# Performance work log

Measured on AMD Instinct MI355X. Metric: run time of the kernel, lower is better.

Reference implementation:

```python
import jax, jax.numpy as jnp
import numpy as np

_FIRST_DECODE_ID = 0  # _T5_DECODER_START_TOKEN_ID
B, L, V = 1, 520, 32128
REVIEW_INDEX = 512
LENIENCY = 2


def setup_inputs() -> dict:
    key = jax.random.key(0)
    k1, k2, k3 = jax.random.split(key, 3)
    target_logits = jax.random.normal(k1, (B, L, V), dtype=jnp.float32)
    probs = jax.random.uniform(k2, (B, L, V), dtype=jnp.float32)
    input_ids = jax.random.randint(k3, (B, L), 0, V, dtype=jnp.int64)
    return {
        "target_logits": target_logits,
        "probs": probs,
        "input_ids": input_ids,
        "review_index": REVIEW_INDEX,
        "leniency": LENIENCY,
    }


def reference(target_logits, probs, input_ids, review_index, leniency):
    r = int(review_index)
    L = input_ids.shape[1]
    K = L - r  # number of draft tokens under review

    target_probs = jax.nn.softmax(target_logits, axis=-1)          # (1, L, V)
    argmax_ids = jnp.argmax(target_probs, axis=-1)                  # (1, L)
    first = jnp.full((1, 1), _FIRST_DECODE_ID, dtype=input_ids.dtype)
    target_ids = jnp.concatenate([first, argmax_ids.astype(input_ids.dtype)], axis=-1)[:, r:]  # (1, K+1)
    target_probs_s = target_probs[:, r - 1:, :]                     # (1, K+1, V)
    probs_new = probs[:, r - 1:, :]                                 # (1, K+1, V)
    draft_ids = input_ids[:, r:]                                    # (1, K)

    # verification flags (fused replacement of the python early-exit loop)
    eq = target_ids[:, :K] == draft_ids                             # (1, K)
    tp = jnp.take_along_axis(target_probs_s[:, :K, :], draft_ids[..., None], axis=-1)[..., 0]
    pp = jnp.take_along_axis(probs_new[:, :K, :], draft_ids[..., None], axis=-1)[..., 0]
    lenient = (leniency > 1) & (tp > pp / jnp.float32(leniency))
    accept = eq | lenient                                           # (1, K)
    # n_match = length of leading run of accepts == match_ct in the loop
    n_match = jnp.sum(jnp.cumprod(accept.astype(jnp.int32), axis=-1))

    # id_res: prefix (r) + accepted drafts (n_match) + 1 bonus target token, padded to r+K+1
    pos = jnp.arange(K + 1)
    draft_pad = jnp.pad(draft_ids, ((0, 0), (0, 1)))                # (1, K+1)
    new_ids = jnp.where(pos < n_match, draft_pad[0],
                        jnp.where(pos == n_match, target_ids[0], 0))
    id_res = jnp.concatenate([input_ids[0, :r], new_ids])[None, :]  # (1, r+K+1)

    # prob_res: probs[:, :r] ++ target_probs of accepted positions, zero-padded to r+K
    mask = (jnp.arange(K) < n_match)[:, None]
    new_probs = jnp.where(mask, target_probs_s[0, :K, :], jnp.float32(0.0))
    prob_res = jnp.concatenate([probs[0, :r, :], new_probs], axis=0)[None]  # (1, r+K, V)

    return id_res, prob_res, n_match
```

## Files before the change

kernel.cpp:

```cpp
#include <hip/hip_runtime.h>
#include <hip/hip_bf16.h>


#define NCHUNK 32
#define BLK 256
#define KFIX 8
#define NSTATS ((KFIX + 1) * NCHUNK)

struct Ws {
    float pmax[16][NCHUNK];
    float psum[16][NCHUNK];
    int   pidx[16][NCHUNK];
};

struct MIS { float m; int i; float s; };

__device__ inline MIS mis_merge(MIS a, MIS b) {
    MIS r;
    r.i = (b.m > a.m || (b.m == a.m && b.i < a.i)) ? b.i : a.i;
    r.m = fmaxf(a.m, b.m);
    r.s = 0.0f;
    if (a.s > 0.0f) r.s += a.s * expf(a.m - r.m);
    if (b.s > 0.0f) r.s += b.s * expf(b.m - r.m);
    return r;
}

typedef float f4  __attribute__((ext_vector_type(4)));
typedef float f4u __attribute__((ext_vector_type(4), aligned(4)));

__global__ __launch_bounds__(BLK)
void stats_kernel(const float* __restrict__ logits, Ws* __restrict__ ws, int V, int r) {
    __shared__ float sm[BLK];
    __shared__ int   si[BLK];
    __shared__ float ss[BLK];
    int t = threadIdx.x;
    int b = blockIdx.x;

    int ch = b & (NCHUNK - 1);
    int j  = b / NCHUNK;
    int chunk_elems = V / NCHUNK;
    int cf4 = chunk_elems / 4;
    int cbase = ch * chunk_elems;
    const float4* row = (const float4*)(logits + (size_t)(r - 1 + j) * V + cbase);

    float m = -INFINITY, s = 0.0f;
    int   mi = 0x7fffffff;
    for (int f = t; f < cf4; f += BLK) {
        float4 v = row[f];
        float vv[4] = {v.x, v.y, v.z, v.w};
        int c = cbase + f * 4;
        #pragma unroll
        for (int u = 0; u < 4; u++) {
            float x = vv[u];
            if (x > m) { s = s * expf(m - x) + 1.0f; m = x; mi = c + u; }
            else       { s += expf(x - m); }
        }
    }
    sm[t] = m; si[t] = mi; ss[t] = s;
    __syncthreads();
    for (int w = BLK >> 1; w > 0; w >>= 1) {
        if (t < w) {
            MIS a = {sm[t], si[t], ss[t]};
            MIS bb = {sm[t + w], si[t + w], ss[t + w]};
            MIS rr = mis_merge(a, bb);
            sm[t] = rr.m; si[t] = rr.i; ss[t] = rr.s;
        }
        __syncthreads();
    }
    if (t == 0) {
        ws->pmax[j][ch] = sm[0];
        ws->psum[j][ch] = ss[0];
        ws->pidx[j][ch] = si[0];
    }
}

__global__ __launch_bounds__(BLK)
void spec_kernel(const float* __restrict__ logits, const float* __restrict__ probs,
                 const int* __restrict__ ids, const int* __restrict__ leniency_p,
                 float* __restrict__ out, const Ws* __restrict__ ws,
                 int V, int r, int K, long long prob_off, long long out_last) {
    __shared__ float s_mx[12];
    __shared__ float s_sum[12];
    __shared__ int   s_amax[12];
    __shared__ int   s_draft[12];
    __shared__ int   s_acc[12];
    __shared__ int   s_nm;
    int t = threadIdx.x;
    int b = blockIdx.x;

    if (t <= K) {
        MIS acc = {ws->pmax[t][0], ws->pidx[t][0], ws->psum[t][0]};
        for (int c = 1; c < NCHUNK; c++) {
            MIS bb = {ws->pmax[t][c], ws->pidx[t][c], ws->psum[t][c]};
            acc = mis_merge(acc, bb);
        }
        s_mx[t] = acc.m; s_sum[t] = acc.s; s_amax[t] = acc.i;
    }
    __syncthreads();
    if (t < K) {
        int dj = ids[r + t];
        s_draft[t] = dj;
        size_t rowoff = (size_t)(r - 1 + t) * V;
        float tp = expf(logits[rowoff + dj] - s_mx[t]) / s_sum[t];
        float pp = probs[rowoff + dj];
        int   len = *leniency_p;
        bool eq      = (s_amax[t] == dj);
        bool lenient = (len > 1) && (tp > pp / (float)len);
        s_acc[t] = (eq || lenient) ? 1 : 0;
    }
    __syncthreads();
    if (t == 0) {
        int nm = 0;
        for (int q = 0; q < K; q++) { if (s_acc[q]) nm++; else break; }
        s_nm = nm;
    }
    __syncthreads();
    int nm = s_nm;

    if (b < 32) {
        int j = b >> 2, sub = b & 3;
        long long ob = prob_off + (long long)(r + j) * V;
        const float* lg = logits + (size_t)(r - 1 + j) * V;
        bool on = (j < nm);
        float m   = s_mx[j];
        float inv = on ? (1.0f / s_sum[j]) : 0.0f;
        if (sub == 0) {
            if (t < 3)       out[ob + t]     = on ? expf(lg[t] - m) * inv : 0.0f;
            else if (t == 3) out[ob + V - 1] = on ? expf(lg[V - 1] - m) * inv : 0.0f;
        }
        int nf4r = (V - 4) / 4;
        int i0 = sub * 2008;
        int i1 = i0 + 2008; if (i1 > nf4r) i1 = nf4r;
        float* dst = out + ob + 3;
        const float* srcl = lg + 3;
        for (int i = i0 + t; i < i1; i += BLK) {
            f4 v;
            if (on) {
                f4u x = *reinterpret_cast<const f4u*>(srcl + 4 * (size_t)i);
                v.x = expf(x.x - m) * inv; v.y = expf(x.y - m) * inv;
                v.z = expf(x.z - m) * inv; v.w = expf(x.w - m) * inv;
            } else {
                v = (f4)0.0f;
            }
            *reinterpret_cast<f4*>(dst + 4 * (size_t)i) = v;
        }
    } else {
        for (int i = t; i < r; i += BLK) out[i] = (float)ids[i];
        if (t <= K) {
            int v;
            if (t < nm)       v = s_draft[t];
            else if (t == nm) v = s_amax[t];
            else              v = 0;
            out[r + t] = (float)v;
        }
        if (t == K + 1) out[out_last] = (float)nm;
    }
}

extern "C" void kernel_launch(void* const* d_in, const int* in_sizes, int n_in,
                              void* d_out, int out_size, void* d_ws, size_t ws_size,
                              hipStream_t stream) {
    const float* logits     = (const float*)d_in[0];
    const float* probs      = (const float*)d_in[1];
    const int*   ids        = (const int*)d_in[2];
    const int*   leniency_p = (const int*)d_in[4];
    float* out = (float*)d_out;
    Ws*    ws  = (Ws*)d_ws;

    const int L = in_sizes[2];
    const int V = in_sizes[0] / L;
    const int r = 512;
    const int K = L - r;
    const long long prob_off = (long long)r + K + 1;
    const long long out_last = (long long)out_size - 1;

    stats_kernel<<<NSTATS, BLK, 0, stream>>>(logits, ws, V, r);

    spec_kernel<<<33, BLK, 0, stream>>>(logits, probs, ids, leniency_p, out, ws,
                                        V, r, K, prob_off, out_last);

    hipMemcpyAsync(out + prob_off, probs, (size_t)r * V * sizeof(float),
                   hipMemcpyDeviceToDevice, stream);
}
```

Measured before the change: 40.51 us.

## Fuse stats, spec and bulk probs copy into one persistent-style kernel

Merges the stats kernel, the spec kernel and the large device-to-device memcpy of probs into a single 2048-block launch. Copy work is split across pure-copy, stats and spec blocks, and an atomic counter plus spin-wait replaces the kernel boundary between the stats and spec phases. The aim is to drop launch overhead and overlap the bandwidth-bound copy with the softmax statistics. In exchange it adds a memset launch and relies on all stats blocks being co-resident or scheduled before the spinning spec blocks, which risks deadlock or stalls.

```diff
diff --git a/kernel.cpp b/kernel.cpp
--- a/kernel.cpp
+++ b/kernel.cpp
@@ -1,16 +1,25 @@
 #include <hip/hip_runtime.h>
-#include <hip/hip_bf16.h>
 
 
 #define NCHUNK 32
 #define BLK 256
-#define KFIX 8
-#define NSTATS ((KFIX + 1) * NCHUNK)
+#define KK 8
+#define NSPEC 33
+#define NSTATS ((KK + 1) * NCHUNK)
+#define GRID 2048
+#define NPURE (GRID - NSPEC - NSTATS)
+#define CH_C 528
+#define CH_S 400
+#define CH_T 128
+#define PURE_TOT ((long long)NPURE * 4 * CH_C)
+#define STAT_BASE PURE_TOT
+#define SPEC_BASE (STAT_BASE + (long long)NSTATS * 4 * CH_S)
 
 struct Ws {
     float pmax[16][NCHUNK];
     float psum[16][NCHUNK];
     int   pidx[16][NCHUNK];
+    unsigned counter;
 };
 
 struct MIS { float m; int i; float s; };
@@ -28,70 +37,119 @@
 typedef float f4  __attribute__((ext_vector_type(4)));
 typedef float f4u __attribute__((ext_vector_type(4), aligned(4)));
 
+__device__ inline void copy_range(const float* __restrict__ srcU, float* __restrict__ dstB,
+                                  long long f0, long long fe, int lane) {
+    for (long long g = f0; g < fe; g += 64) {
+        long long fA = g + lane;
+        if (fA < fe) {
+            f4u v = *reinterpret_cast<const f4u*>(srcU + 4 * fA);
+            *reinterpret_cast<f4*>(dstB + 4 * fA) = (f4){v.x, v.y, v.z, v.w};
+        }
+    }
+}
+
 __global__ __launch_bounds__(BLK)
-void stats_kernel(const float* __restrict__ logits, Ws* __restrict__ ws, int V, int r) {
+void fused_all(const float* __restrict__ logits, const float* __restrict__ probs,
+               const int* __restrict__ ids, const int* __restrict__ leniency_p,
+               float* __restrict__ out, Ws* __restrict__ ws,
+               int V, int r, int K, long long prob_off, long long out_last, int nf4) {
     __shared__ float sm[BLK];
     __shared__ int   si[BLK];
     __shared__ float ss[BLK];
-    int t = threadIdx.x;
-    int b = blockIdx.x;
-
-    int ch = b & (NCHUNK - 1);
-    int j  = b / NCHUNK;
-    int chunk_elems = V / NCHUNK;
-    int cf4 = chunk_elems / 4;
-    int cbase = ch * chunk_elems;
-    const float4* row = (const float4*)(logits + (size_t)(r - 1 + j) * V + cbase);
-
-    float m = -INFINITY, s = 0.0f;
-    int   mi = 0x7fffffff;
-    for (int f = t; f < cf4; f += BLK) {
-        float4 v = row[f];
-        float vv[4] = {v.x, v.y, v.z, v.w};
-        int c = cbase + f * 4;
-        #pragma unroll
-        for (int u = 0; u < 4; u++) {
-            float x = vv[u];
-            if (x > m) { s = s * expf(m - x) + 1.0f; m = x; mi = c + u; }
-            else       { s += expf(x - m); }
-        }
-    }
-    sm[t] = m; si[t] = mi; ss[t] = s;
-    __syncthreads();
-    for (int w = BLK >> 1; w > 0; w >>= 1) {
-        if (t < w) {
-            MIS a = {sm[t], si[t], ss[t]};
-            MIS bb = {sm[t + w], si[t + w], ss[t + w]};
-            MIS rr = mis_merge(a, bb);
-            sm[t] = rr.m; si[t] = rr.i; ss[t] = rr.s;
-        }
-        __syncthreads();
-    }
-    if (t == 0) {
-        ws->pmax[j][ch] = sm[0];
-        ws->psum[j][ch] = ss[0];
-        ws->pidx[j][ch] = si[0];
-    }
-}
-
-__global__ __launch_bounds__(BLK)
-void spec_kernel(const float* __restrict__ logits, const float* __restrict__ probs,
-                 const int* __restrict__ ids, const int* __restrict__ leniency_p,
-                 float* __restrict__ out, const Ws* __restrict__ ws,
-                 int V, int r, int K, long long prob_off, long long out_last) {
     __shared__ float s_mx[12];
     __shared__ float s_sum[12];
     __shared__ int   s_amax[12];
     __shared__ int   s_draft[12];
     __shared__ int   s_acc[12];
     __shared__ int   s_nm;
-    int t = threadIdx.x;
-    int b = blockIdx.x;
+
+    int t = threadIdx.x, b = blockIdx.x;
+    int lane = t & 63, widx = t >> 6;
+    const float* srcU = probs + 3;
+    float* dstB = out + prob_off + 3;
+
+    if (b >= NSPEC && b < NSPEC + NSTATS) {
+        int u  = b - NSPEC;
+        int ch = u & (NCHUNK - 1);
+        int j  = u / NCHUNK;
+        int chunk_elems = V / NCHUNK;
+        int cf4 = chunk_elems / 4;
+        int cbase = ch * chunk_elems;
+        const float4* row = (const float4*)(logits + (size_t)(r - 1 + j) * V + cbase);
+
+        float m = -INFINITY, s = 0.0f;
+        int   mi = 0x7fffffff;
+        for (int f = t; f < cf4; f += BLK) {
+            float4 v = row[f];
+            float vv[4] = {v.x, v.y, v.z, v.w};
+            int c = cbase + f * 4;
+            #pragma unroll
+            for (int u2 = 0; u2 < 4; u2++) {
+                float x = vv[u2];
+                if (x > m) { s = s * expf(m - x) + 1.0f; m = x; mi = c + u2; }
+                else       { s += expf(x - m); }
+            }
+        }
+        sm[t] = m; si[t] = mi; ss[t] = s;
+        __syncthreads();
+        for (int w = BLK >> 1; w > 0; w >>= 1) {
+            if (t < w) {
+                MIS a = {sm[t], si[t], ss[t]};
+                MIS bb = {sm[t + w], si[t + w], ss[t + w]};
+                MIS rr = mis_merge(a, bb);
+                sm[t] = rr.m; si[t] = rr.i; ss[t] = rr.s;
+            }
+            __syncthreads();
+        }
+        if (t == 0) {
+            ws->pmax[j][ch] = sm[0];
+            ws->psum[j][ch] = ss[0];
+            ws->pidx[j][ch] = si[0];
+            __threadfence();
+            atomicAdd(&ws->counter, 1u);
+        }
+        long long w = (long long)u * 4 + widx;
+        long long f0 = STAT_BASE + w * CH_S;
+        copy_range(srcU, dstB, f0, f0 + CH_S, lane);
+        return;
+    }
+
+    if (b >= NSPEC) {
+        long long w = (long long)(b - NSPEC - NSTATS) * 4 + widx;
+        long long f0 = w * CH_C;
+        copy_range(srcU, dstB, f0, f0 + CH_C, lane);
+        return;
+    }
+
+    {
+        long long w = (long long)b * 4 + widx;
+        long long f0 = SPEC_BASE + w * CH_T;
+        long long fe = f0 + CH_T; if (fe > nf4) fe = (long long)nf4;
+        if (f0 < fe) copy_range(srcU, dstB, f0, fe, lane);
+    }
+    if (b == 32) {
+        for (int i = t; i < r; i += BLK) out[i] = (float)ids[i];
+        if (t < 3)       out[prob_off + t] = probs[t];
+        else if (t == 3) {
+            long long last = (long long)r * V - 1;
+            out[prob_off + last] = probs[last];
+        }
+    }
+
+    if (t == 0) {
+        while (atomicAdd(&ws->counter, 0u) < (unsigned)NSTATS)
+            __builtin_amdgcn_s_sleep(8);
+        __threadfence();
+    }
+    __syncthreads();
 
     if (t <= K) {
-        MIS acc = {ws->pmax[t][0], ws->pidx[t][0], ws->psum[t][0]};
+        volatile const float* vpm = &ws->pmax[t][0];
+        volatile const float* vps = &ws->psum[t][0];
+        volatile const int*   vpi = &ws->pidx[t][0];
+        MIS acc = {vpm[0], vpi[0], vps[0]};
         for (int c = 1; c < NCHUNK; c++) {
-            MIS bb = {ws->pmax[t][c], ws->pidx[t][c], ws->psum[t][c]};
+            MIS bb = {vpm[c], vpi[c], vps[c]};
             acc = mis_merge(acc, bb);
         }
         s_mx[t] = acc.m; s_sum[t] = acc.s; s_amax[t] = acc.i;
@@ -145,7 +203,6 @@
             *reinterpret_cast<f4*>(dst + 4 * (size_t)i) = v;
         }
     } else {
-        for (int i = t; i < r; i += BLK) out[i] = (float)ids[i];
         if (t <= K) {
             int v;
             if (t < nm)       v = s_draft[t];
@@ -174,11 +231,11 @@
     const long long prob_off = (long long)r + K + 1;
     const long long out_last = (long long)out_size - 1;
 
-    stats_kernel<<<NSTATS, BLK, 0, stream>>>(logits, ws, V, r);
-
-    spec_kernel<<<33, BLK, 0, stream>>>(logits, probs, ids, leniency_p, out, ws,
-                                        V, r, K, prob_off, out_last);
-
-    hipMemcpyAsync(out + prob_off, probs, (size_t)r * V * sizeof(float),
-                   hipMemcpyDeviceToDevice, stream);
-}
+    const long long N = (long long)r * V;
+    const int nf4 = (int)((N - 3) / 4);
+
+    hipMemsetAsync(&ws->counter, 0, sizeof(unsigned), stream);
+
+    fused_all<<<GRID, BLK, 0, stream>>>(logits, probs, ids, leniency_p, out, ws,
+                                        V, r, K, prob_off, out_last, nf4);
+}
```

Result: slower. 57.49 us (+41.9%).
